# Optimization experiments

Hardware: AMD Instinct MI355X
Metric: run time of the kernel (lower is better)

The kernel has to match this reference:

```python
import jax, jax.numpy as jnp
import numpy as np

B, T, C = 2, 1024, 1024
NH, HS, BD, HORIZON = 16, 64, 16, 64


def setup_inputs() -> dict:
    key = jax.random.key(0)
    ks = jax.random.split(key, 16)
    s = 0.02
    return {
        "x": jax.random.normal(ks[0], (B, T, C), jnp.float32),
        "W_disp": jax.random.normal(ks[1], (NH * BD, C), jnp.float32) * s,
        "b_disp": jnp.zeros((NH * BD,), jnp.float32),
        "W_val": jax.random.normal(ks[2], (C, C), jnp.float32) * s,
        "b_val": jnp.zeros((C,), jnp.float32),
        "rel_pos_emb": jax.random.normal(ks[3], (HORIZON, BD), jnp.float32) * s,
        "W_fused": jax.random.normal(ks[4], (2 * BD, BD), jnp.float32) * s,
        "b_fused": jnp.zeros((2 * BD,), jnp.float32),
        "W_pos": jax.random.normal(ks[5], (BD, BD), jnp.float32) * s,
        "W_bond": jax.random.normal(ks[6], (BD,), jnp.float32) * s,
        "b_bond": jnp.zeros((), jnp.float32),
        "W_dmg": jax.random.normal(ks[7], (BD,), jnp.float32) * s,
        "b_dmg": jnp.full((), -3.0, jnp.float32),  # nn.init.constant_(damage_out.bias, -3.0)
        "W_cproj": jax.random.normal(ks[8], (C, C), jnp.float32) * s,
        "b_cproj": jnp.zeros((C,), jnp.float32),
    }


def reference(x, W_disp, b_disp, W_val, b_val, rel_pos_emb, W_fused, b_fused,
              W_pos, W_bond, b_bond, W_dmg, b_dmg, W_cproj, b_cproj):
    delta = min(HORIZON, T)
    gelu = lambda z: jax.nn.gelu(z, approximate=False)  # torch F.gelu default (erf)

    # projections + head split: (B,nh,T,bd) / (B,nh,T,hs)
    disp = (x @ W_disp.T + b_disp).reshape(B, T, NH, BD).transpose(0, 2, 1, 3)
    val = (x @ W_val.T + b_val).reshape(B, T, NH, HS).transpose(0, 2, 1, 3)

    pad = delta - 1
    disp_pad = jnp.pad(disp, ((0, 0), (0, 0), (pad, 0), (0, 0)))
    idx = jnp.arange(T)[:, None] + jnp.arange(delta)[None, :]  # (T,delta) into padded axis
    disp_win = disp_pad[:, :, idx]                      # (B,nh,T,delta,bd)
    strain = disp_win - disp[:, :, :, None, :]          # bond strain

    fused = strain @ W_fused.T + b_fused                # (B,nh,T,delta,2bd)
    bond_f, dmg_f = fused[..., :BD], fused[..., BD:]
    pos_feat = rel_pos_emb[:delta] @ W_pos.T            # (delta,bd)

    bond_logits = gelu(bond_f + pos_feat) @ W_bond + b_bond          # (B,nh,T,delta)
    damage = jax.nn.sigmoid(gelu(dmg_f) @ W_dmg + b_dmg)             # (B,nh,T,delta)
    logits = bond_logits - 10.0 * damage

    cmask = (jnp.arange(T)[:, None] - delta + 1 + jnp.arange(delta)[None, :]) >= 0
    logits = jnp.where(cmask[None, None], logits, -jnp.inf)
    weights = jax.nn.softmax(logits, axis=-1)           # (B,nh,T,delta)

    # weighted sum over window without materializing (B,nh,T,delta,hs)
    val_pad = jnp.pad(val, ((0, 0), (0, 0), (pad, 0), (0, 0)))
    def body(acc, j):
        sl = jax.lax.dynamic_slice_in_dim(val_pad, j, T, axis=2)  # (B,nh,T,hs)
        return acc + weights[..., j][..., None] * sl, None
    out0 = jnp.zeros((B, NH, T, HS), jnp.float32)
    out, _ = jax.lax.scan(body, out0, jnp.arange(delta))

    y = out.transpose(0, 2, 1, 3).reshape(B, T, C)
    return y @ W_cproj.T + b_cproj
```

## Files before the change

### kernel.cpp

```cpp
#include <hip/hip_runtime.h>

#define BDIM 16
#define HSZ 64
#define NHEAD 16
#define DELTA 64
#define LOG2E 1.4426950408889634f

typedef __bf16 bf16x8 __attribute__((ext_vector_type(8)));
typedef float f32x4 __attribute__((ext_vector_type(4)));
typedef unsigned short us8 __attribute__((ext_vector_type(8)));
typedef unsigned int u32;

__device__ __forceinline__ unsigned short f2bf(float f) {
    u32 u = __float_as_uint(f);
    return (unsigned short)((u + 0x7fffu + ((u >> 16) & 1u)) >> 16);
}
__device__ __forceinline__ float bf2f(unsigned short s) {
    return __uint_as_float(((u32)s) << 16);
}

__device__ __forceinline__ void gload_lds16(const void* g, void* l) {
    __builtin_amdgcn_global_load_lds(
        (const __attribute__((address_space(1))) void*)g,
        (__attribute__((address_space(3))) void*)l, 16, 0, 0);
}

__global__ __launch_bounds__(256) void cast4_bf16(
    const float* __restrict__ s0, unsigned short* __restrict__ d0,
    const float* __restrict__ s1, unsigned short* __restrict__ d1,
    const float* __restrict__ s2, unsigned short* __restrict__ d2,
    const float* __restrict__ s3, unsigned short* __restrict__ d3,
    const float* __restrict__ bd, const float* __restrict__ bv,
    float* __restrict__ bcat) {
    int blk = blockIdx.x;
    if (blk == 4352) {
        for (int t = threadIdx.x; t < 320; t += 256) {
            if (t < 64) ((float4*)bcat)[t] = ((const float4*)bd)[t];
            else        ((float4*)bcat)[t] = ((const float4*)bv)[t - 64];
        }
        return;
    }
    const float* src; unsigned short* dst; int base;
    if (blk < 2048)      { src = s0; dst = d0; base = blk; }
    else if (blk < 2304) { src = s1; dst = d1; base = blk - 2048; }
    else if (blk < 3328) { src = s2; dst = d2; base = blk - 2304; }
    else                 { src = s3; dst = d3; base = blk - 3328; }
    int i = base * 256 + threadIdx.x;
    float4 f = ((const float4*)src)[i];
    ushort4 o;
    o.x = f2bf(f.x); o.y = f2bf(f.y); o.z = f2bf(f.z); o.w = f2bf(f.w);
    ((ushort4*)dst)[i] = o;
}

__global__ __launch_bounds__(256) void gemm_bf16(const unsigned short* __restrict__ A,
                                                 const unsigned short* __restrict__ Bw,
                                                 const float* __restrict__ bias,
                                                 float* __restrict__ C,
                                                 unsigned short* __restrict__ CbT,
                                                 int N, int K, int mode) {
    __shared__ __align__(16) unsigned short lA[2][32 * 512];
    __shared__ __align__(16) unsigned short lB[2][16 * 512];
    int tid = threadIdx.x;
    int w = tid >> 6, lane = tid & 63;
    int bm = blockIdx.y * 128, bn = blockIdx.x * 64;
    int wr = w & 1, wc = w >> 1;
    int m16 = lane & 15, q = lane >> 4;

    const unsigned short* aPtr[8];
    const unsigned short* bPtr[4];
#pragma unroll
    for (int i = 0; i < 8; ++i) {
        int g = w + 4 * i;
        aPtr[i] = A + (long)(bm + (g & 7) * 16 + m16) * K + (g >> 3) * 32 + q * 8;
    }
#pragma unroll
    for (int i = 0; i < 4; ++i) {
        int g = w + 4 * i;
        bPtr[i] = Bw + (long)(bn + (g & 3) * 16 + m16) * K + (g >> 2) * 32 + q * 8;
    }

    f32x4 acc[4][2];
#pragma unroll
    for (int i = 0; i < 4; ++i)
#pragma unroll
        for (int j = 0; j < 2; ++j) acc[i][j] = (f32x4){0.f, 0.f, 0.f, 0.f};

    int nk = K >> 7;
#pragma unroll
    for (int i = 0; i < 8; ++i) gload_lds16(aPtr[i], &lA[0][(w + 4 * i) * 512]);
#pragma unroll
    for (int i = 0; i < 4; ++i) gload_lds16(bPtr[i], &lB[0][(w + 4 * i) * 512]);

    for (int kt = 0; kt < nk; ++kt) {
        int p = kt & 1;
        __syncthreads();
        if (kt + 1 < nk) {
            int ko = (kt + 1) * 128;
#pragma unroll
            for (int i = 0; i < 8; ++i)
                gload_lds16(aPtr[i] + ko, &lA[p ^ 1][(w + 4 * i) * 512]);
#pragma unroll
            for (int i = 0; i < 4; ++i)
                gload_lds16(bPtr[i] + ko, &lB[p ^ 1][(w + 4 * i) * 512]);
        }
#pragma unroll
        for (int s = 0; s < 4; ++s) {
            bf16x8 af[4], bg[2];
#pragma unroll
            for (int r = 0; r < 4; ++r)
                af[r] = *(const bf16x8*)&lA[p][(s * 8 + wr * 4 + r) * 512 + lane * 8];
#pragma unroll
            for (int n = 0; n < 2; ++n)
                bg[n] = *(const bf16x8*)&lB[p][(s * 4 + wc * 2 + n) * 512 + lane * 8];
#pragma unroll
            for (int r = 0; r < 4; ++r)
#pragma unroll
                for (int n = 0; n < 2; ++n)
                    acc[r][n] = __builtin_amdgcn_mfma_f32_16x16x32_bf16(af[r], bg[n], acc[r][n], 0, 0, 0);
        }
    }

    if (mode == 0 || bn < 256) {
        int ldc = (mode == 0) ? N : 256;
#pragma unroll
        for (int n = 0; n < 2; ++n) {
            int col = bn + wc * 32 + n * 16 + m16;
            float bv = bias[col];
#pragma unroll
            for (int r = 0; r < 4; ++r)
#pragma unroll
                for (int e = 0; e < 4; ++e) {
                    int row = bm + wr * 64 + r * 16 + q * 4 + e;
                    C[(long)row * ldc + col] = acc[r][n][e] + bv;
                }
        }
    } else {
        __syncthreads();
        unsigned short* sC = (unsigned short*)&lA[0][0];
#pragma unroll
        for (int n = 0; n < 2; ++n) {
            int col_l = wc * 32 + n * 16 + m16;
            float bv = bias[bn + col_l];
#pragma unroll
            for (int r = 0; r < 4; ++r)
#pragma unroll
                for (int e = 0; e < 4; ++e) {
                    int row_l = wr * 64 + r * 16 + q * 4 + e;
                    sC[row_l * 64 + col_l] = f2bf(acc[r][n][e] + bv);
                }
        }
        __syncthreads();
        int hs = tid & 63, tq = tid >> 6;
        long base = ((long)(bm >> 10)) * 1048576 + (long)(bn - 256 + hs) * 1024 + (bm & 1023);
#pragma unroll
        for (int it = 0; it < 4; ++it) {
            int t = tq * 32 + it * 8;
            us8 o;
#pragma unroll
            for (int j = 0; j < 8; ++j) o[j] = sC[(t + j) * 64 + hs];
            *(us8*)&CbT[base + t] = o;
        }
    }
}

__device__ __forceinline__ float gelu_p(float z) {
    float z2 = z * z;
    float u = z * __builtin_fmaf(0.0356774081f, z2, 0.7978845608f);
    float u2 = u * u;
    float num = u * (15.f + u2);
    float den = __builtin_fmaf(6.f, u2, 15.f);
    float th = num * __builtin_amdgcn_rcpf(den);
    float zh = 0.5f * z;
    return __builtin_fmaf(zh, th, zh);
}

#define PROJ_LD 36
#define VW_LD 136

__global__ __launch_bounds__(512) void attn_kernel(
    const float* __restrict__ disp,
    const unsigned short* __restrict__ valT,
    const float* __restrict__ rel,
    const float* __restrict__ Wpos,
    const float* __restrict__ Wf,
    const float* __restrict__ bfu,
    const float* __restrict__ Wb,
    const float* __restrict__ bb_p,
    const float* __restrict__ Wd,
    const float* __restrict__ bd_p,
    unsigned short* __restrict__ y,
    int T) {
    __shared__ __align__(16) unsigned short sWd[64 * VW_LD];
    __shared__ __align__(16) float ov[128 * PROJ_LD + 128 * 16 + 512];
    float* sProj = ov;
    float* sDisp = ov + 128 * PROJ_LD;
    float* sWfT  = sDisp + 128 * 16;
    unsigned short* sValT = (unsigned short*)ov;

    int tid = threadIdx.x;
    int ntile = T / 64;
    int t0 = (blockIdx.x % ntile) * 64;
    int bh = blockIdx.x / ntile;
    int b = bh / NHEAD, h = bh % NHEAD;
    int wave = tid >> 6, lane = tid & 63;
    int m16 = lane & 15, q = lane >> 4;

    {
        uint4 z4 = make_uint4(0, 0, 0, 0);
        for (int i = tid; i < 1088; i += 512) ((uint4*)sWd)[i] = z4;
        if (tid < 512) sWfT[(tid & 15) * 32 + (tid >> 4)] = Wf[tid];
        {
            int r = tid >> 2, qq = tid & 3;
            int ts = t0 + r - 64;
            float4 v = make_float4(0.f, 0.f, 0.f, 0.f);
            if (ts >= 0)
                v = ((const float4*)(disp + ((long)(b * T + ts) * NHEAD + h) * BDIM))[qq];
            *(float4*)&sDisp[r * 16 + qq * 4] = v;
        }
    }
    __syncthreads();
    for (int idx = tid; idx < 128 * 32; idx += 512) {
        int r = idx >> 5, k = idx & 31;
        float a = 0.f;
#pragma unroll
        for (int d = 0; d < 16; ++d) a += sDisp[r * 16 + d] * sWfT[d * 32 + k];
        sProj[r * PROJ_LD + k] = a;
    }

    float relv[16];
#pragma unroll
    for (int e = 0; e < 4; ++e) {
        float4 rr = ((const float4*)rel)[lane * 4 + e];
        relv[e * 4 + 0] = rr.x; relv[e * 4 + 1] = rr.y;
        relv[e * 4 + 2] = rr.z; relv[e * 4 + 3] = rr.w;
    }
    float pfr[16], pdr[16], wbr[16], wdr[16];
#pragma unroll
    for (int d = 0; d < 16; ++d) {
        float a = 0.f;
#pragma unroll
        for (int e = 0; e < 16; ++e) a += relv[e] * Wpos[d * 16 + e];
        pfr[d] = a + bfu[d];
        pdr[d] = bfu[16 + d];
        wbr[d] = Wb[d];
        wdr[d] = Wd[d];
    }
    float bbond = *bb_p, bdmg = *bd_p;
    __syncthreads();

    int wbase = wave * 8;
    for (int rr = 0; rr < 8; ++rr) {
        int tl = wbase + rr;
        int rs = tl + 1 + lane;
        int rc = tl + 64;
        bool valid = (t0 + tl + lane - 63) >= 0;
        float cb[16], cd[16], pb[16], pd[16];
        const float* crow = &sProj[rc * PROJ_LD];
        const float* prow = &sProj[rs * PROJ_LD];
#pragma unroll
        for (int qq = 0; qq < 4; ++qq) {
            float4 v1 = *(const float4*)&crow[qq * 4];
            float4 v2 = *(const float4*)&crow[16 + qq * 4];
            float4 v3 = *(const float4*)&prow[qq * 4];
            float4 v4 = *(const float4*)&prow[16 + qq * 4];
            cb[qq*4+0]=v1.x; cb[qq*4+1]=v1.y; cb[qq*4+2]=v1.z; cb[qq*4+3]=v1.w;
            cd[qq*4+0]=v2.x; cd[qq*4+1]=v2.y; cd[qq*4+2]=v2.z; cd[qq*4+3]=v2.w;
            pb[qq*4+0]=v3.x; pb[qq*4+1]=v3.y; pb[qq*4+2]=v3.z; pb[qq*4+3]=v3.w;
            pd[qq*4+0]=v4.x; pd[qq*4+1]=v4.y; pd[qq*4+2]=v4.z; pd[qq*4+3]=v4.w;
        }
        float bl = bbond, dm = bdmg;
#pragma unroll
        for (int k = 0; k < 16; ++k) {
            bl = __builtin_fmaf(gelu_p(pb[k] - cb[k] + pfr[k]), wbr[k], bl);
            dm = __builtin_fmaf(gelu_p(pd[k] - cd[k] + pdr[k]), wdr[k], dm);
        }
        float damage = __builtin_amdgcn_rcpf(1.f + __builtin_exp2f(-dm * LOG2E));
        float logit = bl - 10.f * damage;
        if (!valid) logit = -1e30f;
        float mx = logit;
#pragma unroll
        for (int off = 32; off >= 1; off >>= 1) mx = fmaxf(mx, __shfl_xor(mx, off));
        float e = __builtin_exp2f((logit - mx) * LOG2E);
        float ssum = e;
#pragma unroll
        for (int off = 32; off >= 1; off >>= 1) ssum += __shfl_xor(ssum, off);
        sWd[tl * VW_LD + rs] = f2bf(e * __builtin_amdgcn_rcpf(ssum));
    }
    __syncthreads();

    {
        int hs = lane;
        long vbase = ((long)(b * NHEAD * HSZ + h * HSZ + hs)) * T + (t0 - 64);
#pragma unroll
        for (int it = 0; it < 2; ++it) {
            int g = wave * 2 + it;
            int ts0 = t0 - 64 + g * 8;
            us8 v = (us8)0;
            if (ts0 >= 0) v = *(const us8*)&valT[vbase + g * 8];
            *(us8*)&sValT[hs * VW_LD + g * 8] = v;
        }
    }
    __syncthreads();

    {
        int mi = wave >> 1;
        int nh = (wave & 1) * 2;
        int kt0 = mi >> 1;
        f32x4 acc[2];
#pragma unroll
        for (int n = 0; n < 2; ++n) acc[n] = (f32x4){0.f, 0.f, 0.f, 0.f};
#pragma unroll
        for (int kk = 0; kk < 3; ++kk) {
            int kt = kt0 + kk;
            bf16x8 a = *(const bf16x8*)&sWd[(mi * 16 + m16) * VW_LD + kt * 32 + q * 8];
#pragma unroll
            for (int n = 0; n < 2; ++n) {
                bf16x8 bv = *(const bf16x8*)&sValT[((nh + n) * 16 + m16) * VW_LD + kt * 32 + q * 8];
                acc[n] = __builtin_amdgcn_mfma_f32_16x16x32_bf16(a, bv, acc[n], 0, 0, 0);
            }
        }
        int trow = t0 + mi * 16 + q * 4;
#pragma unroll
        for (int n = 0; n < 2; ++n) {
            int col = h * HSZ + (nh + n) * 16 + m16;
#pragma unroll
            for (int e = 0; e < 4; ++e)
                y[(long)(b * T + trow + e) * (NHEAD * HSZ) + col] = f2bf(acc[n][e]);
        }
    }
}

extern "C" void kernel_launch(void* const* d_in, const int* in_sizes, int n_in,
                              void* d_out, int out_size, void* d_ws, size_t ws_size,
                              hipStream_t stream) {
    const float* x       = (const float*)d_in[0];
    const float* W_disp  = (const float*)d_in[1];
    const float* b_disp  = (const float*)d_in[2];
    const float* W_val   = (const float*)d_in[3];
    const float* b_val   = (const float*)d_in[4];
    const float* rel     = (const float*)d_in[5];
    const float* W_fused = (const float*)d_in[6];
    const float* b_fused = (const float*)d_in[7];
    const float* W_pos   = (const float*)d_in[8];
    const float* W_bond  = (const float*)d_in[9];
    const float* b_bond  = (const float*)d_in[10];
    const float* W_dmg   = (const float*)d_in[11];
    const float* b_dmg   = (const float*)d_in[12];
    const float* W_cproj = (const float*)d_in[13];
    const float* b_cproj = (const float*)d_in[14];
    float* out = (float*)d_out;
    float* ws  = (float*)d_ws;

    const int B = 2, T = 1024, C = 1024;
    float* disp = ws;
    float* bcat = disp + 524288;
    unsigned short* x_bf  = (unsigned short*)(bcat + 1280);
    unsigned short* valT  = x_bf + 2097152;
    unsigned short* Wcat  = valT + 2097152;
    unsigned short* Wv_bf = Wcat + 262144;
    unsigned short* Wc_bf = Wv_bf + 1048576;
    unsigned short* y_bf  = x_bf;

    cast4_bf16<<<4353, 256, 0, stream>>>(x, x_bf, W_disp, Wcat, W_val, Wv_bf,
                                         W_cproj, Wc_bf, b_disp, b_val, bcat);

    gemm_bf16<<<dim3(20, 16), 256, 0, stream>>>(x_bf, Wcat, bcat, disp, valT,
                                                1280, C, 1);
    attn_kernel<<<dim3(B * NHEAD * (T / 64)), 512, 0, stream>>>(
        disp, valT, rel, W_pos, W_fused, b_fused, W_bond, b_bond, W_dmg, b_dmg,
        y_bf, T);
    gemm_bf16<<<dim3(16, 16), 256, 0, stream>>>(y_bf, Wc_bf, b_cproj, out, nullptr,
                                                C, C, 0);
}
```

Baseline: 190.7 us.

## Shrink GEMM tiles to 64x64 and remap blocks per XCD

```diff
diff --git a/kernel.cpp b/kernel.cpp
--- a/kernel.cpp
+++ b/kernel.cpp
@@ -57,63 +57,62 @@
                                                  const float* __restrict__ bias,
                                                  float* __restrict__ C,
                                                  unsigned short* __restrict__ CbT,
-                                                 int N, int K, int mode) {
-    __shared__ __align__(16) unsigned short lA[2][32 * 512];
-    __shared__ __align__(16) unsigned short lB[2][16 * 512];
+                                                 int N, int K, int nbx, int mode) {
+    __shared__ __align__(16) unsigned short lA[2][8 * 512];
+    __shared__ __align__(16) unsigned short lB[2][8 * 512];
     int tid = threadIdx.x;
     int w = tid >> 6, lane = tid & 63;
-    int bm = blockIdx.y * 128, bn = blockIdx.x * 64;
+    int id = blockIdx.x;
+    int xcd = id & 7, rr = id >> 3;
+    int mi = xcd * 4 + (rr & 3);
+    int ni = rr >> 2;
+    int bm = mi * 64, bn = ni * 64;
     int wr = w & 1, wc = w >> 1;
     int m16 = lane & 15, q = lane >> 4;
 
-    const unsigned short* aPtr[8];
-    const unsigned short* bPtr[4];
-#pragma unroll
-    for (int i = 0; i < 8; ++i) {
+    const unsigned short* aPtr[2];
+    const unsigned short* bPtr[2];
+#pragma unroll
+    for (int i = 0; i < 2; ++i) {
         int g = w + 4 * i;
-        aPtr[i] = A + (long)(bm + (g & 7) * 16 + m16) * K + (g >> 3) * 32 + q * 8;
-    }
-#pragma unroll
-    for (int i = 0; i < 4; ++i) {
-        int g = w + 4 * i;
+        aPtr[i] = A + (long)(bm + (g & 3) * 16 + m16) * K + (g >> 2) * 32 + q * 8;
         bPtr[i] = Bw + (long)(bn + (g & 3) * 16 + m16) * K + (g >> 2) * 32 + q * 8;
     }
 
-    f32x4 acc[4][2];
-#pragma unroll
-    for (int i = 0; i < 4; ++i)
+    f32x4 acc[2][2];
+#pragma unroll
+    for (int i = 0; i < 2; ++i)
 #pragma unroll
         for (int j = 0; j < 2; ++j) acc[i][j] = (f32x4){0.f, 0.f, 0.f, 0.f};
 
-    int nk = K >> 7;
-#pragma unroll
-    for (int i = 0; i < 8; ++i) gload_lds16(aPtr[i], &lA[0][(w + 4 * i) * 512]);
-#pragma unroll
-    for (int i = 0; i < 4; ++i) gload_lds16(bPtr[i], &lB[0][(w + 4 * i) * 512]);
+    int nk = K >> 6;
+#pragma unroll
+    for (int i = 0; i < 2; ++i) {
+        gload_lds16(aPtr[i], &lA[0][(w + 4 * i) * 512]);
+        gload_lds16(bPtr[i], &lB[0][(w + 4 * i) * 512]);
+    }
 
     for (int kt = 0; kt < nk; ++kt) {
         int p = kt & 1;
         __syncthreads();
         if (kt + 1 < nk) {
-            int ko = (kt + 1) * 128;
-#pragma unroll
-            for (int i = 0; i < 8; ++i)
+            int ko = (kt + 1) * 64;
+#pragma unroll
+            for (int i = 0; i < 2; ++i) {
                 gload_lds16(aPtr[i] + ko, &lA[p ^ 1][(w + 4 * i) * 512]);
-#pragma unroll
-            for (int i = 0; i < 4; ++i)
                 gload_lds16(bPtr[i] + ko, &lB[p ^ 1][(w + 4 * i) * 512]);
-        }
-#pragma unroll
-        for (int s = 0; s < 4; ++s) {
-            bf16x8 af[4], bg[2];
-#pragma unroll
-            for (int r = 0; r < 4; ++r)
-                af[r] = *(const bf16x8*)&lA[p][(s * 8 + wr * 4 + r) * 512 + lane * 8];
-#pragma unroll
-            for (int n = 0; n < 2; ++n)
-                bg[n] = *(const bf16x8*)&lB[p][(s * 4 + wc * 2 + n) * 512 + lane * 8];
-#pragma unroll
-            for (int r = 0; r < 4; ++r)
+            }
+        }
+#pragma unroll
+        for (int s = 0; s < 2; ++s) {
+            bf16x8 af[2], bg[2];
+#pragma unroll
+            for (int r = 0; r < 2; ++r) {
+                af[r] = *(const bf16x8*)&lA[p][(s * 4 + wr * 2 + r) * 512 + lane * 8];
+                bg[r] = *(const bf16x8*)&lB[p][(s * 4 + wc * 2 + r) * 512 + lane * 8];
+            }
+#pragma unroll
+            for (int r = 0; r < 2; ++r)
 #pragma unroll
                 for (int n = 0; n < 2; ++n)
                     acc[r][n] = __builtin_amdgcn_mfma_f32_16x16x32_bf16(af[r], bg[n], acc[r][n], 0, 0, 0);
@@ -127,10 +126,10 @@
             int col = bn + wc * 32 + n * 16 + m16;
             float bv = bias[col];
 #pragma unroll
-            for (int r = 0; r < 4; ++r)
+            for (int r = 0; r < 2; ++r)
 #pragma unroll
                 for (int e = 0; e < 4; ++e) {
-                    int row = bm + wr * 64 + r * 16 + q * 4 + e;
+                    int row = bm + wr * 32 + r * 16 + q * 4 + e;
                     C[(long)row * ldc + col] = acc[r][n][e] + bv;
                 }
         }
@@ -142,10 +141,10 @@
             int col_l = wc * 32 + n * 16 + m16;
             float bv = bias[bn + col_l];
 #pragma unroll
-            for (int r = 0; r < 4; ++r)
+            for (int r = 0; r < 2; ++r)
 #pragma unroll
                 for (int e = 0; e < 4; ++e) {
-                    int row_l = wr * 64 + r * 16 + q * 4 + e;
+                    int row_l = wr * 32 + r * 16 + q * 4 + e;
                     sC[row_l * 64 + col_l] = f2bf(acc[r][n][e] + bv);
                 }
         }
@@ -153,8 +152,8 @@
         int hs = tid & 63, tq = tid >> 6;
         long base = ((long)(bm >> 10)) * 1048576 + (long)(bn - 256 + hs) * 1024 + (bm & 1023);
 #pragma unroll
-        for (int it = 0; it < 4; ++it) {
-            int t = tq * 32 + it * 8;
+        for (int it = 0; it < 2; ++it) {
+            int t = tq * 16 + it * 8;
             us8 o;
 #pragma unroll
             for (int j = 0; j < 8; ++j) o[j] = sC[(t + j) * 64 + hs];
@@ -364,11 +363,11 @@
     cast4_bf16<<<4353, 256, 0, stream>>>(x, x_bf, W_disp, Wcat, W_val, Wv_bf,
                                          W_cproj, Wc_bf, b_disp, b_val, bcat);
 
-    gemm_bf16<<<dim3(20, 16), 256, 0, stream>>>(x_bf, Wcat, bcat, disp, valT,
-                                                1280, C, 1);
+    gemm_bf16<<<640, 256, 0, stream>>>(x_bf, Wcat, bcat, disp, valT,
+                                       1280, C, 20, 1);
     attn_kernel<<<dim3(B * NHEAD * (T / 64)), 512, 0, stream>>>(
         disp, valT, rel, W_pos, W_fused, b_fused, W_bond, b_bond, W_dmg, b_dmg,
         y_bf, T);
-    gemm_bf16<<<dim3(16, 16), 256, 0, stream>>>(y_bf, Wc_bf, b_cproj, out, nullptr,
-                                                C, C, 0);
-}
+    gemm_bf16<<<512, 256, 0, stream>>>(y_bf, Wc_bf, b_cproj, out, nullptr,
+                                       C, C, 16, 0);
+}
```

Result: faster. 175.5 us (-8.0%).
